# Optimization experiments

Measured on AMD Instinct MI355X. Metric: run time of the kernel, lower is better.

## Reference

```python
import jax, jax.numpy as jnp
import numpy as np

HEADS = 4
LN_EPS = 1e-5

def layernorm(x, w, b):
    m = x.mean(-1, keepdims=True)
    v = ((x - m) ** 2).mean(-1, keepdims=True)
    return (x - m) * jax.lax.rsqrt(v + LN_EPS) * w + b

def conv3d(x, w, b, pad, dil=1, groups=1):
    out = jax.lax.conv_general_dilated(
        x, w, (1, 1, 1), [(pad, pad)] * 3,
        rhs_dilation=(dil, dil, dil),
        dimension_numbers=('NCDHW', 'OIDHW', 'NCDHW'),
        feature_group_count=groups)
    return out + b[None, :, None, None, None]

def trilinear_gather(x_flat, pz, py, px, D, H, W):
    # x_flat: [B,C,S]; pz/py/px: [B,S] fractional sample coords, zero padding outside
    z0f, y0f, x0f = jnp.floor(pz), jnp.floor(py), jnp.floor(px)
    wz, wy, wx = pz - z0f, py - y0f, px - x0f
    z0, y0, x0 = z0f.astype(jnp.int32), y0f.astype(jnp.int32), x0f.astype(jnp.int32)
    acc = jnp.zeros_like(x_flat)
    for dz in (0, 1):
        for dy in (0, 1):
            for dx in (0, 1):
                iz, iy, ix = z0 + dz, y0 + dy, x0 + dx
                cw = (wz if dz else 1.0 - wz) * (wy if dy else 1.0 - wy) * (wx if dx else 1.0 - wx)
                valid = (iz >= 0) & (iz < D) & (iy >= 0) & (iy < H) & (ix >= 0) & (ix < W)
                idx = (jnp.clip(iz, 0, D - 1) * H + jnp.clip(iy, 0, H - 1)) * W + jnp.clip(ix, 0, W - 1)
                vals = jnp.take_along_axis(x_flat, idx[:, None, :], axis=2)
                acc = acc + vals * (cw * valid)[:, None, :]
    return acc

def deform_conv3d(x, off_w, off_b, w, b):
    # DeformConvPack: offsets from a regular 3x3x3 conv, then offset trilinear sampling + conv
    B, C, D, H, W = x.shape
    K = 27
    offsets = conv3d(x, off_w, off_b, 1).reshape(B, K, 3, D * H * W)
    gz, gy, gx = jnp.indices((D, H, W))
    bz = gz.reshape(-1).astype(x.dtype)[None]
    by = gy.reshape(-1).astype(x.dtype)[None]
    bx = gx.reshape(-1).astype(x.dtype)[None]
    x_flat = x.reshape(B, C, -1)
    O = w.shape[0]
    wk = w.reshape(O, C, K)
    out = jnp.zeros((B, O, D * H * W), x.dtype)
    for k in range(K):  # fixed 27 kernel taps
        kz, ky, kx = k // 9, (k // 3) % 3, k % 3
        pz = bz + (kz - 1) + offsets[:, k, 0]
        py = by + (ky - 1) + offsets[:, k, 1]
        px = bx + (kx - 1) + offsets[:, k, 2]
        samp = trilinear_gather(x_flat, pz, py, px, D, H, W)  # [B,C,S]
        out = out + jnp.einsum('bcs,oc->bos', samp, wk[:, :, k])
    out = out + b[None, :, None]
    return out.reshape(B, O, D, H, W)

def forward(x, temperature, qkv_w, norm_w, norm_b, proj1_w, proj1_b, conv0_w, conv0_b,
            convsp_w, convsp_b, off_w, off_b, dcn_w, dcn_b, conv1_w, conv1_b,
            proj2_w, proj2_b, norm2_w, norm2_b, out_w, out_b, H, W, D):
    B, N, C = x.shape
    hd = C // HEADS
    qkv = (x @ qkv_w.T).reshape(B, N, 3, HEADS, hd).transpose(2, 0, 3, 1, 4)  # [3,B,h,N,hd]
    q = qkv[0].transpose(0, 1, 3, 2)  # [B,h,hd,N]
    k = qkv[1].transpose(0, 1, 3, 2)
    v = qkv[2].transpose(0, 1, 3, 2)
    q = q / jnp.maximum(jnp.sqrt((q * q).sum(-1, keepdims=True)), 1e-12)
    k = k / jnp.maximum(jnp.sqrt((k * k).sum(-1, keepdims=True)), 1e-12)
    attn = jnp.einsum('bhcn,bhdn->bhcd', q, k) * temperature[None]
    attn = jax.nn.softmax(attn, axis=-1)
    x_ca = jnp.einsum('bhcd,bhdn->bhcn', attn, v).transpose(0, 3, 1, 2).reshape(B, N, C)
    x_ca = layernorm(x_ca, norm_w, norm_b)
    x5 = x_ca.transpose(0, 2, 1).reshape(B, C, H, W, D)
    shortcut = x5
    y = jnp.einsum('bcxyz,oc->boxyz', x5, proj1_w) + proj1_b[None, :, None, None, None]
    y = jax.nn.gelu(y, approximate=False)
    u = y
    a = conv3d(y, conv0_w, conv0_b, 2, 1, C)      # depthwise k=5 pad=2
    a = conv3d(a, convsp_w, convsp_b, 9, 3, C)    # depthwise k=7 pad=9 dil=3
    a = deform_conv3d(a, off_w, off_b, dcn_w, dcn_b)
    a = jnp.einsum('bcxyz,oc->boxyz', a, conv1_w) + conv1_b[None, :, None, None, None]
    y = u * a
    y = jnp.einsum('bcxyz,oc->boxyz', y, proj2_w) + proj2_b[None, :, None, None, None]
    y = y + shortcut
    x_sa = y.reshape(B, C, N).transpose(0, 2, 1)           # lka returns [B,N,C]
    x_sa = x_sa.reshape(B, C, N).transpose(0, 2, 1)        # faithful torch reshape-after-permute
    x_sa = layernorm(x_sa, norm2_w, norm2_b)
    return x_sa @ out_w.T + out_b

def setup_inputs():
    key = jax.random.key(0)
    ks = jax.random.split(key, 12)
    B, C, H, W, D = 2, 64, 32, 32, 32
    N = H * W * D
    s = 0.02
    return dict(
        x=jax.random.normal(ks[0], (B, N, C), jnp.float32),
        temperature=jnp.ones((HEADS, 1, 1), jnp.float32),
        qkv_w=jax.random.normal(ks[1], (3 * C, C), jnp.float32) * s,
        norm_w=jnp.ones((C,), jnp.float32), norm_b=jnp.zeros((C,), jnp.float32),
        proj1_w=jax.random.normal(ks[2], (C, C), jnp.float32) * s,
        proj1_b=jnp.zeros((C,), jnp.float32),
        conv0_w=jax.random.normal(ks[3], (C, 1, 5, 5, 5), jnp.float32) * s,
        conv0_b=jnp.zeros((C,), jnp.float32),
        convsp_w=jax.random.normal(ks[4], (C, 1, 7, 7, 7), jnp.float32) * s,
        convsp_b=jnp.zeros((C,), jnp.float32),
        off_w=jax.random.normal(ks[5], (81, C, 3, 3, 3), jnp.float32) * 0.01,
        off_b=jnp.zeros((81,), jnp.float32),
        dcn_w=jax.random.normal(ks[6], (C, C, 3, 3, 3), jnp.float32) * s,
        dcn_b=jnp.zeros((C,), jnp.float32),
        conv1_w=jax.random.normal(ks[7], (C, C), jnp.float32) * s,
        conv1_b=jnp.zeros((C,), jnp.float32),
        proj2_w=jax.random.normal(ks[8], (C, C), jnp.float32) * s,
        proj2_b=jnp.zeros((C,), jnp.float32),
        norm2_w=jnp.ones((C,), jnp.float32), norm2_b=jnp.zeros((C,), jnp.float32),
        out_w=jax.random.normal(ks[9], (C, C), jnp.float32) * s,
        out_b=jnp.zeros((C,), jnp.float32),
        B_in=B, C_in=C, H=H, W=W, D=D,
    )

def reference(x, temperature, qkv_w, norm_w, norm_b, proj1_w, proj1_b, conv0_w, conv0_b,
              convsp_w, convsp_b, off_w, off_b, dcn_w, dcn_b, conv1_w, conv1_b,
              proj2_w, proj2_b, norm2_w, norm2_b, out_w, out_b, B_in, C_in, H, W, D):
    return forward(x, temperature, qkv_w, norm_w, norm_b, proj1_w, proj1_b, conv0_w, conv0_b,
                   convsp_w, convsp_b, off_w, off_b, dcn_w, dcn_b, conv1_w, conv1_b,
                   proj2_w, proj2_b, norm2_w, norm2_b, out_w, out_b, H, W, D)
```

## Files before the change

### kernel.cpp

```cpp
#include <hip/hip_runtime.h>
#include <hip/hip_bf16.h>

#define S 32768
#define BUFN (2*64*32768)

typedef __bf16 v8bf __attribute__((ext_vector_type(8)));
typedef float v4f __attribute__((ext_vector_type(4)));
typedef int v4i __attribute__((ext_vector_type(4)));

__device__ __forceinline__ ushort f2b(float f) {
  union { float f; unsigned u; } v; v.f = f;
  unsigned r = (v.u + 0x7fffu + ((v.u >> 16) & 1u)) >> 16;
  return (ushort)r;
}
__device__ __forceinline__ float b2f(ushort h) {
  union { unsigned u; float f; } v; v.u = ((unsigned)h) << 16;
  return v.f;
}
__device__ __forceinline__ float u2f(unsigned u) {
  union { unsigned u; float f; } v; v.u = u;
  return v.f;
}
__device__ __forceinline__ v8bf pack8(const float* f) {
  v4i d;
#pragma unroll
  for (int m = 0; m < 4; m++)
    d[m] = (int)((unsigned)f2b(f[2*m]) | ((unsigned)f2b(f[2*m+1]) << 16));
  return __builtin_bit_cast(v8bf, d);
}

__global__ void k_wt(const float* __restrict__ offw, const float* __restrict__ dcnw,
                     const float* __restrict__ qkvw, const float* __restrict__ p1w,
                     const float* __restrict__ c1w, const float* __restrict__ p2w,
                     ushort* __restrict__ wt_off16, ushort* __restrict__ wt_dcn16,
                     ushort* __restrict__ qkv16, ushort* __restrict__ p1w16,
                     ushort* __restrict__ c1w16, ushort* __restrict__ p2w16) {
  int i = blockIdx.x*256 + threadIdx.x;
  if (i < 27*96*64) {
    int c = i & 63, o = (i >> 6) % 96, t = i / 6144;
    wt_off16[i] = (o < 81) ? f2b(offw[o*1728 + c*27 + t]) : (ushort)0;
  }
  if (i < 27*64*64) {
    int c = i & 63, o = (i >> 6) & 63, k = i >> 12;
    wt_dcn16[i] = f2b(dcnw[(o*64 + c)*27 + k]);
  }
  if (i < 12288) qkv16[i] = f2b(qkvw[i]);
  if (i < 4096) {
    p1w16[i] = f2b(p1w[i]);
    c1w16[i] = f2b(c1w[i]);
    p2w16[i] = f2b(p2w[i]);
  }
}

__global__ __launch_bounds__(256) void k_qkv(const float* __restrict__ x,
    const ushort* __restrict__ qkvw16, float* __restrict__ q,
    float* __restrict__ k, float* __restrict__ v) {
  int bi = blockIdx.x;
  int b = bi >> 9, tile = bi & 511;
  int tid = threadIdx.x;
  int lane = tid & 63, wv = tid >> 6;
  int si = lane & 15, rq = lane >> 4, q8 = rq << 3;
  int s = (tile << 6) + (wv << 4) + si;
  const float* xr = x + ((size_t)(b*S + s) << 6);
  float4 t0 = *(const float4*)(xr + q8);
  float4 t1 = *(const float4*)(xr + q8 + 4);
  float4 t2 = *(const float4*)(xr + q8 + 32);
  float4 t3 = *(const float4*)(xr + q8 + 36);
  float f0[8] = {t0.x,t0.y,t0.z,t0.w,t1.x,t1.y,t1.z,t1.w};
  float f1[8] = {t2.x,t2.y,t2.z,t2.w,t3.x,t3.y,t3.z,t3.w};
  v8bf b0 = pack8(f0);
  v8bf b1 = pack8(f1);
  v4f acc[12];
#pragma unroll
  for (int t = 0; t < 12; t++) acc[t] = (v4f){0.f,0.f,0.f,0.f};
#pragma unroll
  for (int t = 0; t < 12; t++) {
    const ushort* ap = qkvw16 + (((t<<4) + si) << 6) + q8;
    v8bf a0 = *(const v8bf*)ap;
    v8bf a1 = *(const v8bf*)(ap + 32);
    acc[t] = __builtin_amdgcn_mfma_f32_16x16x32_bf16(a0, b0, acc[t], 0,0,0);
    acc[t] = __builtin_amdgcn_mfma_f32_16x16x32_bf16(a1, b1, acc[t], 0,0,0);
  }
#pragma unroll
  for (int t = 0; t < 12; t++) {
    float* dst = (t < 4) ? q : (t < 8 ? k : v);
    int chb = (t & 3) << 4;
#pragma unroll
    for (int r = 0; r < 4; r++) {
      int ch = chb + rq*4 + r;
      dst[((size_t)(b*64 + ch))*S + s] = acc[t][r];
    }
  }
}

__global__ __launch_bounds__(256) void k_rownorm(const float* __restrict__ q,
    const float* __restrict__ k, float* __restrict__ inv) {
  int row = blockIdx.x;
  const float* p = (row < 128) ? (q + (size_t)row*S) : (k + (size_t)(row-128)*S);
  const float4* p4 = (const float4*)p;
  float ss = 0.f;
  for (int i = threadIdx.x; i < S/4; i += 256) {
    float4 t = p4[i];
    ss += t.x*t.x + t.y*t.y + t.z*t.z + t.w*t.w;
  }
  __shared__ float red[256];
  red[threadIdx.x] = ss; __syncthreads();
  for (int st = 128; st > 0; st >>= 1) {
    if (threadIdx.x < st) red[threadIdx.x] += red[threadIdx.x+st];
    __syncthreads();
  }
  if (threadIdx.x == 0) inv[row] = 1.0f / fmaxf(sqrtf(red[0]), 1e-12f);
}

__global__ __launch_bounds__(256) void k_gram(const float* __restrict__ q,
    const float* __restrict__ k, float* __restrict__ gram) {
  int bi = blockIdx.x;
  int b = bi >> 8, h = (bi >> 6) & 3, chunk = bi & 63;
  int tid = threadIdx.x;
  int lane = tid & 63, wv = tid >> 6;
  int si = lane & 15, rq = lane >> 4, q8 = rq << 3;
  const float* qb = q + ((size_t)(b*64 + h*16 + si))*S;
  const float* kb = k + ((size_t)(b*64 + h*16 + si))*S;
  int n0 = chunk*512 + wv*128;
  v4f acc = (v4f){0.f,0.f,0.f,0.f};
#pragma unroll
  for (int st = 0; st < 4; st++) {
    int n = n0 + st*32 + q8;
    float4 qa = *(const float4*)(qb + n);
    float4 qc = *(const float4*)(qb + n + 4);
    float4 ka = *(const float4*)(kb + n);
    float4 kc = *(const float4*)(kb + n + 4);
    float fq[8] = {qa.x,qa.y,qa.z,qa.w,qc.x,qc.y,qc.z,qc.w};
    float fk[8] = {ka.x,ka.y,ka.z,ka.w,kc.x,kc.y,kc.z,kc.w};
    v8bf a0 = pack8(fq);
    v8bf b0 = pack8(fk);
    acc = __builtin_amdgcn_mfma_f32_16x16x32_bf16(a0, b0, acc, 0,0,0);
  }
#pragma unroll
  for (int r = 0; r < 4; r++) {
    int c = rq*4 + r;
    atomicAdd(&gram[((b*4+h)*16 + c)*16 + si], acc[r]);
  }
}

__global__ __launch_bounds__(256) void k_xca_ln(const float* __restrict__ v,
    const float* __restrict__ gram, const float* __restrict__ inv,
    const float* __restrict__ temp,
    const float* __restrict__ nw, const float* __restrict__ nb,
    float* __restrict__ x5) {
  __shared__ float at[1024];
  __shared__ float wsh[64], bsh[64];
  int gid = blockIdx.x*256 + threadIdx.x;
  int b = gid >> 15, n = gid & (S-1);
  int tid = threadIdx.x;
  if (tid < 64) {
    int h = tid >> 4, c = tid & 15;
    float iq = inv[b*64 + h*16 + c];
    float tp = temp[h];
    float l[16], m = -1e30f;
#pragma unroll
    for (int d = 0; d < 16; d++) {
      float vv = gram[((b*4+h)*16+c)*16 + d] * iq * inv[128 + b*64 + h*16 + d] * tp;
      l[d] = vv; m = fmaxf(m, vv);
    }
    float s = 0.f;
#pragma unroll
    for (int d = 0; d < 16; d++) { l[d] = expf(l[d]-m); s += l[d]; }
    float is = 1.0f / s;
#pragma unroll
    for (int d = 0; d < 16; d++) at[(h*16+c)*16 + d] = l[d]*is;
  } else if (tid < 128) {
    wsh[tid-64] = nw[tid-64]; bsh[tid-64] = nb[tid-64];
  }
  __syncthreads();
  const float* vb = v + (size_t)b*64*S + n;
  float vv[64];
#pragma unroll
  for (int ch = 0; ch < 64; ch++) vv[ch] = vb[(size_t)ch*S];
  float xc[64];
#pragma unroll
  for (int h = 0; h < 4; h++)
#pragma unroll
    for (int cc = 0; cc < 16; cc++) {
      float a = 0.f;
#pragma unroll
      for (int d = 0; d < 16; d++) a += at[(h*16+cc)*16 + d] * vv[h*16+d];
      xc[h*16+cc] = a;
    }
  float mean = 0.f;
#pragma unroll
  for (int ch = 0; ch < 64; ch++) mean += xc[ch];
  mean *= (1.0f/64.0f);
  float var = 0.f;
#pragma unroll
  for (int ch = 0; ch < 64; ch++) { float d = xc[ch]-mean; var += d*d; }
  var *= (1.0f/64.0f);
  float rs = rsqrtf(var + 1e-5f);
  float* xb = x5 + (size_t)b*64*S + n;
#pragma unroll
  for (int ch = 0; ch < 64; ch++)
    xb[(size_t)ch*S] = (xc[ch]-mean)*rs*wsh[ch] + bsh[ch];
}

__global__ __launch_bounds__(256) void k_proj1(const float* __restrict__ x5,
    const ushort* __restrict__ p1w16, const float* __restrict__ bias, float* __restrict__ u) {
  int bi = blockIdx.x;
  int b = bi >> 9, tile = bi & 511;
  int tid = threadIdx.x;
  int lane = tid & 63, wv = tid >> 6;
  int si = lane & 15, rq = lane >> 4, q8 = rq << 3;
  int s = (tile << 6) + (wv << 4) + si;
  const float* xb = x5 + ((size_t)b << 21) + s;
  float f0[8], f1[8];
#pragma unroll
  for (int j = 0; j < 8; j++) {
    f0[j] = xb[(size_t)(q8 + j) << 15];
    f1[j] = xb[(size_t)(32 + q8 + j) << 15];
  }
  v8bf b0 = pack8(f0);
  v8bf b1 = pack8(f1);
  v4f acc[4];
#pragma unroll
  for (int t = 0; t < 4; t++) acc[t] = (v4f){0.f,0.f,0.f,0.f};
#pragma unroll
  for (int t = 0; t < 4; t++) {
    const ushort* ap = p1w16 + (((t<<4) + si) << 6) + q8;
    v8bf a0 = *(const v8bf*)ap;
    v8bf a1 = *(const v8bf*)(ap + 32);
    acc[t] = __builtin_amdgcn_mfma_f32_16x16x32_bf16(a0, b0, acc[t], 0,0,0);
    acc[t] = __builtin_amdgcn_mfma_f32_16x16x32_bf16(a1, b1, acc[t], 0,0,0);
  }
  float* ub = u + ((size_t)b << 21) + s;
#pragma unroll
  for (int t = 0; t < 4; t++)
#pragma unroll
    for (int r = 0; r < 4; r++) {
      int ch = (t << 4) + rq*4 + r;
      float a = acc[t][r] + bias[ch];
      float g = 0.5f*a*(1.0f + erff(a*0.70710678118654752f));
      ub[(size_t)ch << 15] = g;
    }
}

__global__ __launch_bounds__(256) void k_conv0(const float* __restrict__ in,
    const float* __restrict__ w, const float* __restrict__ bias, ushort* __restrict__ out) {
  __shared__ ushort tile[5*32*40];
  __shared__ float wsh[128];
  int bi = blockIdx.x;
  int z = bi & 31, c = (bi >> 5) & 63, b = bi >> 11;
  const float* ib = in + ((size_t)(b*64+c) << 15);
  for (int i = threadIdx.x; i < 800; i += 256)
    ((int4*)tile)[i] = make_int4(0,0,0,0);
  if (threadIdx.x < 125) wsh[threadIdx.x] = w[c*125 + threadIdx.x];
  __syncthreads();
  for (int i = threadIdx.x; i < 5*1024; i += 256) {
    int dz = i >> 10, r = i & 1023;
    int zg = z + dz - 2;
    if (zg >= 0 && zg < 32)
      tile[(dz*32 + (r >> 5))*40 + (r & 31) + 2] = f2b(ib[zg*1024 + r]);
  }
  __syncthreads();
  int y = threadIdx.x >> 3, x0 = (threadIdx.x & 7) << 2;
  float bv = bias[c];
  float acc[4] = {bv, bv, bv, bv};
  for (int dz = 0; dz < 5; dz++) {
#pragma unroll
    for (int dy = 0; dy < 5; dy++) {
      int yy = y + dy - 2;
      if (yy < 0 || yy >= 32) continue;
      const float* wp = &wsh[(dz*5+dy)*5];
      float wreg[5];
#pragma unroll
      for (int dx = 0; dx < 5; dx++) wreg[dx] = wp[dx];
      const ushort* rp = &tile[(dz*32+yy)*40 + x0];
      int2 rl = *(const int2*)rp;
      int2 rh = *(const int2*)(rp + 4);
      float row[8];
      row[0]=u2f(((unsigned)rl.x)<<16); row[1]=u2f(rl.x & 0xffff0000u);
      row[2]=u2f(((unsigned)rl.y)<<16); row[3]=u2f(rl.y & 0xffff0000u);
      row[4]=u2f(((unsigned)rh.x)<<16); row[5]=u2f(rh.x & 0xffff0000u);
      row[6]=u2f(((unsigned)rh.y)<<16); row[7]=u2f(rh.y & 0xffff0000u);
#pragma unroll
      for (int dx = 0; dx < 5; dx++)
#pragma unroll
        for (int j = 0; j < 4; j++)
          acc[j] += wreg[dx] * row[dx+j];
    }
  }
  ushort* ob = out + ((size_t)(b*64+c) << 15) + z*1024 + y*32 + x0;
  unsigned p0 = (unsigned)f2b(acc[0]) | ((unsigned)f2b(acc[1]) << 16);
  unsigned p1 = (unsigned)f2b(acc[2]) | ((unsigned)f2b(acc[3]) << 16);
  *(int2*)ob = make_int2((int)p0, (int)p1);
}

__global__ __launch_bounds__(256) void k_convsp(const ushort* __restrict__ in,
    const float* __restrict__ w, const float* __restrict__ bias, ushort* __restrict__ out) {
  __shared__ ushort tile[7*32*56];
  __shared__ float wsh[344];
  int bi = blockIdx.x;
  int z = bi & 31, c = (bi >> 5) & 63, b = bi >> 11;
  const ushort* ib = in + ((size_t)(b*64+c) << 15);
  for (int i = threadIdx.x; i < 1568; i += 256)
    ((int4*)tile)[i] = make_int4(0,0,0,0);
  for (int i = threadIdx.x; i < 343; i += 256) wsh[i] = w[c*343 + i];
  __syncthreads();
  for (int i = threadIdx.x; i < 7*1024; i += 256) {
    int t = i >> 10, r = i & 1023;
    int zg = z + 3*t - 9;
    if (zg >= 0 && zg < 32)
      tile[(t*32 + (r >> 5))*56 + (r & 31) + 9] = ib[zg*1024 + r];
  }
  __syncthreads();
  int y = threadIdx.x >> 3, x0 = (threadIdx.x & 7) << 2;
  float bv = bias[c];
  float acc[4] = {bv, bv, bv, bv};
  for (int t = 0; t < 7; t++) {
#pragma unroll
    for (int dy = 0; dy < 7; dy++) {
      int yy = y + 3*dy - 9;
      if (yy < 0 || yy >= 32) continue;
      const float* wp = &wsh[(t*7+dy)*7];
      float wreg[7];
#pragma unroll
      for (int dx = 0; dx < 7; dx++) wreg[dx] = wp[dx];
      const ushort* rp = &tile[(t*32+yy)*56 + x0];
      float row[24];
#pragma unroll
      for (int qq = 0; qq < 6; qq++) {
        int2 rv = *(const int2*)(rp + 4*qq);
        row[4*qq+0]=u2f(((unsigned)rv.x)<<16); row[4*qq+1]=u2f(rv.x & 0xffff0000u);
        row[4*qq+2]=u2f(((unsigned)rv.y)<<16); row[4*qq+3]=u2f(rv.y & 0xffff0000u);
      }
#pragma unroll
      for (int dx = 0; dx < 7; dx++)
#pragma unroll
        for (int j = 0; j < 4; j++)
          acc[j] += wreg[dx] * row[3*dx+j];
    }
  }
  ushort* ob = out + ((size_t)(b*64+c) << 15) + z*1024 + y*32 + x0;
  unsigned p0 = (unsigned)f2b(acc[0]) | ((unsigned)f2b(acc[1]) << 16);
  unsigned p1 = (unsigned)f2b(acc[2]) | ((unsigned)f2b(acc[3]) << 16);
  *(int2*)ob = make_int2((int)p0, (int)p1);
}

__global__ __launch_bounds__(256) void k_tr(const ushort* __restrict__ a2,
                                            ushort* __restrict__ a2t) {
  __shared__ ushort tile[64*66];
  int bi = blockIdx.x;
  int b = bi >> 9, chunk = bi & 511;
  int s0 = chunk << 6;
  const ushort* ib = a2 + ((size_t)b << 21) + s0;
#pragma unroll
  for (int i = 0; i < 16; i++) {
    int j = threadIdx.x + (i << 8);
    int c = j >> 6, sl = j & 63;
    tile[c*66 + sl] = ib[((size_t)c << 15) + sl];
  }
  __syncthreads();
  ushort* ob = a2t + ((size_t)b << 21) + ((size_t)s0 << 6);
#pragma unroll
  for (int i = 0; i < 16; i++) {
    int j = threadIdx.x + (i << 8);
    int sl = j >> 6, c = j & 63;
    ob[sl*64 + c] = tile[c*66 + sl];
  }
}

__global__ __launch_bounds__(256) void k_offconv(const ushort* __restrict__ a2t,
    const ushort* __restrict__ wt16, float* __restrict__ off) {
  int bi = blockIdx.x;
  int b = bi >> 9, tile = bi & 511;
  int s0 = tile << 6;
  int tid = threadIdx.x;
  int lane = tid & 63, wv = tid >> 6;
  int si = lane & 15, rq = lane >> 4, q8 = rq << 3;
  int sw = s0 + (wv << 4);
  int s_c = sw + si;
  int zc = s_c >> 10, yc = (s_c >> 5) & 31, xc = s_c & 31;
  const ushort* a2b = a2t + ((size_t)b << 21);
  v4f acc[6];
#pragma unroll
  for (int i = 0; i < 6; i++) acc[i] = (v4f){0.f,0.f,0.f,0.f};
  const v4i z4 = {0,0,0,0};
  for (int t = 0; t < 27; t++) {
    int kz = t/9, ky = (t/3)%3, kx = t%3;
    int zz = zc + kz - 1, yy = yc + ky - 1, xx = xc + kx - 1;
    bool ok = (zz>=0 && zz<32 && yy>=0 && yy<32 && xx>=0 && xx<32);
    v8bf b0 = __builtin_bit_cast(v8bf, z4);
    v8bf b1 = __builtin_bit_cast(v8bf, z4);
    if (ok) {
      const ushort* p = a2b + ((size_t)((zz<<10)+(yy<<5)+xx) << 6) + q8;
      b0 = *(const v8bf*)p;
      b1 = *(const v8bf*)(p + 32);
    }
    const ushort* wk = wt16 + t*6144;
#pragma unroll
    for (int ot = 0; ot < 6; ot++) {
      const ushort* ap = wk + (((ot<<4) + si) << 6) + q8;
      v8bf a0 = *(const v8bf*)ap;
      v8bf a1 = *(const v8bf*)(ap + 32);
      acc[ot] = __builtin_amdgcn_mfma_f32_16x16x32_bf16(a0, b0, acc[ot], 0,0,0);
      acc[ot] = __builtin_amdgcn_mfma_f32_16x16x32_bf16(a1, b1, acc[ot], 0,0,0);
    }
  }
#pragma unroll
  for (int ot = 0; ot < 6; ot++)
#pragma unroll
    for (int r = 0; r < 4; r++) {
      int o = ot*16 + rq*4 + r;
      if (o < 81)
        off[(((size_t)(b*81 + o)) << 15) + sw + si] = acc[ot][r];
    }
}

__global__ __launch_bounds__(256) void k_dcn(const ushort* __restrict__ a2t,
    const float* __restrict__ off, const float* __restrict__ off_b,
    const ushort* __restrict__ wt16, float* __restrict__ out) {
  __shared__ float ofs[81*66];
  __shared__ ushort scr[4][16*72];
  int bi = blockIdx.x;
  int b = bi >> 9, tile = bi & 511;
  int s0 = tile << 6;
  int tid = threadIdx.x;
  const float* offbase = off + (((size_t)(b*81)) << 15) + s0;
  for (int i = tid; i < 5184; i += 256) {
    int r = i >> 6, sl = i & 63;
    ofs[r*66 + sl] = offbase[((size_t)r << 15) + sl] + off_b[r];
  }
  __syncthreads();
  int lane = tid & 63, wv = tid >> 6;
  int sr = lane >> 3, cs = lane & 7;
  int si = lane & 15, rq = lane >> 4;
  int sw = s0 + (wv << 4);
  const ushort* a2b = a2t + ((size_t)b << 21);
  ushort* myscr = &scr[wv][0];
  int sA = sw + sr, sB = sw + 8 + sr;
  int zA = sA >> 10, yA = (sA >> 5) & 31, xA = sA & 31;
  int zB = sB >> 10, yB = (sB >> 5) & 31, xB = sB & 31;
  int slcA = (wv << 4) + sr, slcB = slcA + 8;
  v4f acc[4];
#pragma unroll
  for (int t = 0; t < 4; t++) acc[t] = (v4f){0.f,0.f,0.f,0.f};
  for (int k = 0; k < 27; k++) {
    int kz = k/9, ky = (k/3)%3, kx = k%3;
    int idxA[8], idxB[8];
    float wA[8], wB[8];
    {
      float pz = (float)(zA + kz - 1) + ofs[(3*k+0)*66 + slcA];
      float py = (float)(yA + ky - 1) + ofs[(3*k+1)*66 + slcA];
      float px = (float)(xA + kx - 1) + ofs[(3*k+2)*66 + slcA];
      float fz = floorf(pz), fy = floorf(py), fx = floorf(px);
      float wz = pz-fz, wy = py-fy, wx = px-fx;
      int z0 = (int)fz, y0 = (int)fy, x0 = (int)fx;
      int zi[2], yi[2], xi[2]; float zw[2], yw[2], xw[2];
#pragma unroll
      for (int d = 0; d < 2; d++) {
        int iz = z0 + d; zi[d] = min(max(iz,0),31) << 10;
        zw[d] = (iz >= 0 && iz < 32) ? (d ? wz : 1.f-wz) : 0.f;
        int iy = y0 + d; yi[d] = min(max(iy,0),31) << 5;
        yw[d] = (iy >= 0 && iy < 32) ? (d ? wy : 1.f-wy) : 0.f;
        int ix = x0 + d; xi[d] = min(max(ix,0),31);
        xw[d] = (ix >= 0 && ix < 32) ? (d ? wx : 1.f-wx) : 0.f;
      }
#pragma unroll
      for (int r = 0; r < 8; r++) {
        int dz = r >> 2, dy = (r >> 1) & 1, dx = r & 1;
        idxA[r] = zi[dz] + yi[dy] + xi[dx];
        wA[r] = zw[dz] * yw[dy] * xw[dx];
      }
    }
    {
      float pz = (float)(zB + kz - 1) + ofs[(3*k+0)*66 + slcB];
      float py = (float)(yB + ky - 1) + ofs[(3*k+1)*66 + slcB];
      float px = (float)(xB + kx - 1) + ofs[(3*k+2)*66 + slcB];
      float fz = floorf(pz), fy = floorf(py), fx = floorf(px);
      float wz = pz-fz, wy = py-fy, wx = px-fx;
      int z0 = (int)fz, y0 = (int)fy, x0 = (int)fx;
      int zi[2], yi[2], xi[2]; float zw[2], yw[2], xw[2];
#pragma unroll
      for (int d = 0; d < 2; d++) {
        int iz = z0 + d; zi[d] = min(max(iz,0),31) << 10;
        zw[d] = (iz >= 0 && iz < 32) ? (d ? wz : 1.f-wz) : 0.f;
        int iy = y0 + d; yi[d] = min(max(iy,0),31) << 5;
        yw[d] = (iy >= 0 && iy < 32) ? (d ? wy : 1.f-wy) : 0.f;
        int ix = x0 + d; xi[d] = min(max(ix,0),31);
        xw[d] = (ix >= 0 && ix < 32) ? (d ? wx : 1.f-wx) : 0.f;
      }
#pragma unroll
      for (int r = 0; r < 8; r++) {
        int dz = r >> 2, dy = (r >> 1) & 1, dx = r & 1;
        idxB[r] = zi[dz] + yi[dy] + xi[dx];
        wB[r] = zw[dz] * yw[dy] * xw[dx];
      }
    }
    v4i gA[8], gB[8];
#pragma unroll
    for (int r = 0; r < 8; r++)
      gA[r] = *(const v4i*)(a2b + ((size_t)idxA[r] << 6) + (cs << 3));
#pragma unroll
    for (int r = 0; r < 8; r++)
      gB[r] = *(const v4i*)(a2b + ((size_t)idxB[r] << 6) + (cs << 3));
    float faA[8], faB[8];
#pragma unroll
    for (int j = 0; j < 8; j++) { faA[j] = 0.f; faB[j] = 0.f; }
#pragma unroll
    for (int r = 0; r < 8; r++) {
      float wa = wA[r], wb = wB[r];
#pragma unroll
      for (int m = 0; m < 4; m++) {
        unsigned da = (unsigned)gA[r][m];
        faA[2*m]   += wa * u2f(da << 16);
        faA[2*m+1] += wa * u2f(da & 0xffff0000u);
        unsigned db = (unsigned)gB[r][m];
        faB[2*m]   += wb * u2f(db << 16);
        faB[2*m+1] += wb * u2f(db & 0xffff0000u);
      }
    }
    v4i dA, dB;
#pragma unroll
    for (int m = 0; m < 4; m++) {
      unsigned l0 = (__float_as_uint(faA[2*m])   + 0x8000u) >> 16;
      unsigned h0 = (__float_as_uint(faA[2*m+1]) + 0x8000u) & 0xffff0000u;
      dA[m] = (int)(l0 | h0);
      unsigned l1 = (__float_as_uint(faB[2*m])   + 0x8000u) >> 16;
      unsigned h1 = (__float_as_uint(faB[2*m+1]) + 0x8000u) & 0xffff0000u;
      dB[m] = (int)(l1 | h1);
    }
    *(v4i*)&myscr[sr*72 + (cs << 3)]       = dA;
    *(v4i*)&myscr[(8+sr)*72 + (cs << 3)]   = dB;
    v8bf bf0 = *(const v8bf*)&myscr[si*72 + (rq << 3)];
    v8bf bf1 = *(const v8bf*)&myscr[si*72 + 32 + (rq << 3)];
    const ushort* wk = wt16 + (k << 12);
#pragma unroll
    for (int ot = 0; ot < 4; ot++) {
      const ushort* ap = wk + (((ot<<4) + si) << 6) + (rq << 3);
      v8bf a0 = *(const v8bf*)ap;
      v8bf a1 = *(const v8bf*)(ap + 32);
      acc[ot] = __builtin_amdgcn_mfma_f32_16x16x32_bf16(a0, bf0, acc[ot], 0,0,0);
      acc[ot] = __builtin_amdgcn_mfma_f32_16x16x32_bf16(a1, bf1, acc[ot], 0,0,0);
    }
  }
#pragma unroll
  for (int ot = 0; ot < 4; ot++)
#pragma unroll
    for (int r = 0; r < 4; r++) {
      int o = (ot << 4) + rq*4 + r;
      out[(((size_t)(b*64 + o)) << 15) + sw + si] = acc[ot][r];
    }
}

__global__ __launch_bounds__(256) void k_fuse2(const float* __restrict__ dcn0,
    const float* __restrict__ dcn_b, const ushort* __restrict__ c1w16,
    const float* __restrict__ c1b, const float* __restrict__ u,
    const ushort* __restrict__ p2w16, const float* __restrict__ p2b,
    const float* __restrict__ x5, float* __restrict__ y2) {
  __shared__ ushort scr[4][16*72];
  int bi = blockIdx.x;
  int b = bi >> 9, tile = bi & 511;
  int tid = threadIdx.x;
  int lane = tid & 63, wv = tid >> 6;
  int si = lane & 15, rq = lane >> 4, q8 = rq << 3;
  int s = (tile << 6) + (wv << 4) + si;
  ushort* myscr = &scr[wv][0];
  const float* db = dcn0 + ((size_t)b << 21) + s;
  float f0[8], f1[8];
#pragma unroll
  for (int j = 0; j < 8; j++) {
    f0[j] = db[(size_t)(q8 + j) << 15]      + dcn_b[q8 + j];
    f1[j] = db[(size_t)(32 + q8 + j) << 15] + dcn_b[32 + q8 + j];
  }
  v8bf b0 = pack8(f0);
  v8bf b1 = pack8(f1);
  v4f acc1[4];
#pragma unroll
  for (int t = 0; t < 4; t++) acc1[t] = (v4f){0.f,0.f,0.f,0.f};
#pragma unroll
  for (int t = 0; t < 4; t++) {
    const ushort* ap = c1w16 + (((t<<4) + si) << 6) + q8;
    v8bf a0 = *(const v8bf*)ap;
    v8bf a1 = *(const v8bf*)(ap + 32);
    acc1[t] = __builtin_amdgcn_mfma_f32_16x16x32_bf16(a0, b0, acc1[t], 0,0,0);
    acc1[t] = __builtin_amdgcn_mfma_f32_16x16x32_bf16(a1, b1, acc1[t], 0,0,0);
  }
  const float* ub = u + ((size_t)b << 21) + s;
#pragma unroll
  for (int t = 0; t < 4; t++)
#pragma unroll
    for (int r = 0; r < 4; r++) {
      int o = (t << 4) + rq*4 + r;
      float m = ub[(size_t)o << 15] * (acc1[t][r] + c1b[o]);
      myscr[si*72 + o] = f2b(m);
    }
  v8bf m0 = *(const v8bf*)&myscr[si*72 + q8];
  v8bf m1 = *(const v8bf*)&myscr[si*72 + 32 + q8];
  v4f acc2[4];
#pragma unroll
  for (int t = 0; t < 4; t++) acc2[t] = (v4f){0.f,0.f,0.f,0.f};
#pragma unroll
  for (int t = 0; t < 4; t++) {
    const ushort* ap = p2w16 + (((t<<4) + si) << 6) + q8;
    v8bf a0 = *(const v8bf*)ap;
    v8bf a1 = *(const v8bf*)(ap + 32);
    acc2[t] = __builtin_amdgcn_mfma_f32_16x16x32_bf16(a0, m0, acc2[t], 0,0,0);
    acc2[t] = __builtin_amdgcn_mfma_f32_16x16x32_bf16(a1, m1, acc2[t], 0,0,0);
  }
  const float* sb = x5 + ((size_t)b << 21) + s;
  float* yb = y2 + ((size_t)b << 21) + s;
#pragma unroll
  for (int t = 0; t < 4; t++)
#pragma unroll
    for (int r = 0; r < 4; r++) {
      int o = (t << 4) + rq*4 + r;
      yb[(size_t)o << 15] = acc2[t][r] + p2b[o] + sb[(size_t)o << 15];
    }
}

__global__ __launch_bounds__(256) void k_final(const float* __restrict__ y2,
    const float* __restrict__ n2w, const float* __restrict__ n2b,
    const float* __restrict__ ow, const float* __restrict__ ob, float* __restrict__ out) {
  __shared__ float wsh[4096];
  __shared__ float nw[64], nb[64], obs[64];
  int bi = blockIdx.x;
  int b = bi >> 7; int mg = (bi >> 4) & 7; int r0 = (bi & 15)*4;
  for (int i = threadIdx.x; i < 4096; i += 256) wsh[i] = ow[i];
  if (threadIdx.x < 64) {
    nw[threadIdx.x]=n2w[threadIdx.x]; nb[threadIdx.x]=n2b[threadIdx.x];
    obs[threadIdx.x]=ob[threadIdx.x];
  }
  __syncthreads();
  int mi = threadIdx.x & 63, rg = threadIdx.x >> 6;
  int r = r0 + rg;
  int m = mg*64 + mi;
  int n = m*64 + r;
  const float* yb = y2 + ((size_t)(b*64+r))*S + m;
  float v[64];
#pragma unroll
  for (int c = 0; c < 64; c++) v[c] = yb[(size_t)c*512];
  float mean = 0.f;
#pragma unroll
  for (int c = 0; c < 64; c++) mean += v[c];
  mean *= (1.0f/64.0f);
  float var = 0.f;
#pragma unroll
  for (int c = 0; c < 64; c++) { float d = v[c]-mean; var += d*d; }
  var *= (1.0f/64.0f);
  float rs = rsqrtf(var + 1e-5f);
#pragma unroll
  for (int c = 0; c < 64; c++) v[c] = (v[c]-mean)*rs*nw[c] + nb[c];
  float* orow = out + ((size_t)b*S + n)*64;
  for (int o4 = 0; o4 < 16; o4++) {
    const float4* w0 = (const float4*)&wsh[(o4*4+0)*64];
    const float4* w1 = (const float4*)&wsh[(o4*4+1)*64];
    const float4* w2 = (const float4*)&wsh[(o4*4+2)*64];
    const float4* w3 = (const float4*)&wsh[(o4*4+3)*64];
    float t0=obs[o4*4+0], t1=obs[o4*4+1], t2=obs[o4*4+2], t3=obs[o4*4+3];
#pragma unroll
    for (int c4 = 0; c4 < 16; c4++) {
      float4 a0 = w0[c4], a1 = w1[c4], a2 = w2[c4], a3 = w3[c4];
      float v0 = v[4*c4], v1 = v[4*c4+1], v2 = v[4*c4+2], v3 = v[4*c4+3];
      t0 += a0.x*v0 + a0.y*v1 + a0.z*v2 + a0.w*v3;
      t1 += a1.x*v0 + a1.y*v1 + a1.z*v2 + a1.w*v3;
      t2 += a2.x*v0 + a2.y*v1 + a2.z*v2 + a2.w*v3;
      t3 += a3.x*v0 + a3.y*v1 + a3.z*v2 + a3.w*v3;
    }
    float4 a; a.x=t0; a.y=t1; a.z=t2; a.w=t3;
    ((float4*)orow)[o4] = a;
  }
}

extern "C" void kernel_launch(void* const* d_in, const int* in_sizes, int n_in,
                              void* d_out, int out_size, void* d_ws, size_t ws_size,
                              hipStream_t stream) {
  const float* x      = (const float*)d_in[0];
  const float* temp   = (const float*)d_in[1];
  const float* qkv_w  = (const float*)d_in[2];
  const float* norm_w = (const float*)d_in[3];
  const float* norm_b = (const float*)d_in[4];
  const float* p1w    = (const float*)d_in[5];
  const float* p1b    = (const float*)d_in[6];
  const float* c0w    = (const float*)d_in[7];
  const float* c0b    = (const float*)d_in[8];
  const float* cspw   = (const float*)d_in[9];
  const float* cspb   = (const float*)d_in[10];
  const float* offw   = (const float*)d_in[11];
  const float* offb   = (const float*)d_in[12];
  const float* dcnw   = (const float*)d_in[13];
  const float* dcnb   = (const float*)d_in[14];
  const float* c1w    = (const float*)d_in[15];
  const float* c1b    = (const float*)d_in[16];
  const float* p2w    = (const float*)d_in[17];
  const float* p2b    = (const float*)d_in[18];
  const float* n2w    = (const float*)d_in[19];
  const float* n2b    = (const float*)d_in[20];
  const float* outw   = (const float*)d_in[21];
  const float* outb   = (const float*)d_in[22];
  float* out = (float*)d_out;

  float* Wa  = (float*)d_ws;
  float* Wb  = Wa + BUFN;
  float* Wc  = Wb + BUFN;
  float* OFF = Wc + BUFN;
  float* SM  = OFF + (size_t)2*81*S;
  float* SM_inv  = SM;
  float* SM_gram = SM + 256;
  ushort* WT_OFF16 = (ushort*)(SM + 4352);
  ushort* WT_DCN16 = WT_OFF16 + 165888;
  ushort* QKV16    = WT_DCN16 + 110592;
  ushort* P1W16    = QKV16 + 12288;
  ushort* C1W16    = P1W16 + 4096;
  ushort* P2W16    = C1W16 + 4096;
  float* vbuf = out;
  ushort* A1_16 = (ushort*)d_out;
  ushort* A2_16 = (ushort*)Wc;
  ushort* a2t = (ushort*)d_out;

  hipMemsetAsync(SM, 0, 4352*sizeof(float), stream);
  k_wt     <<<648, 256, 0, stream>>>(offw, dcnw, qkv_w, p1w, c1w, p2w,
                                     WT_OFF16, WT_DCN16, QKV16, P1W16, C1W16, P2W16);

  k_qkv    <<<1024,256, 0, stream>>>(x, QKV16, Wa, Wb, vbuf);
  k_rownorm<<<256, 256, 0, stream>>>(Wa, Wb, SM_inv);
  k_gram   <<<512, 256, 0, stream>>>(Wa, Wb, SM_gram);
  k_xca_ln <<<256, 256, 0, stream>>>(vbuf, SM_gram, SM_inv, temp, norm_w, norm_b, Wa);
  k_proj1  <<<1024,256, 0, stream>>>(Wa, P1W16, p1b, Wb);
  k_conv0  <<<4096,256, 0, stream>>>(Wb, c0w, c0b, A1_16);
  k_convsp <<<4096,256, 0, stream>>>(A1_16, cspw, cspb, A2_16);
  k_tr     <<<1024,256, 0, stream>>>(A2_16, a2t);
  k_offconv<<<1024,256, 0, stream>>>(a2t, WT_OFF16, OFF);
  k_dcn    <<<1024,256, 0, stream>>>(a2t, OFF, offb, WT_DCN16, Wc);
  k_fuse2  <<<1024,256, 0, stream>>>(Wc, dcnb, C1W16, c1b, Wb, P2W16, p2b, Wa, OFF);
  k_final  <<<256, 256, 0, stream>>>(OFF, n2w, n2b, outw, outb, out);
}
```

Measured before the change: 733.8 us.

## Fuse row norms into gram kernel and proj1 into XCA-LN kernel

Row sum-of-squares for q and k are now accumulated inside the gram kernel through shuffles and atomics, which removes the separate rownorm pass over q and k. The proj1 GEMM+GELU is fused into the XCA+LayerNorm kernel: normalized values are staged as bf16 in shared memory and fed straight to MFMA, so x5 is not re-read from global. The memset is folded into the weight-conversion kernel. Risks are extra shared memory (about 37KB) lowering occupancy and a larger register footprint. The x5 output is still written, possibly for a later residual.

```diff
diff --git a/kernel.cpp b/kernel.cpp
--- a/kernel.cpp
+++ b/kernel.cpp
@@ -34,7 +34,8 @@
                      const float* __restrict__ c1w, const float* __restrict__ p2w,
                      ushort* __restrict__ wt_off16, ushort* __restrict__ wt_dcn16,
                      ushort* __restrict__ qkv16, ushort* __restrict__ p1w16,
-                     ushort* __restrict__ c1w16, ushort* __restrict__ p2w16) {
+                     ushort* __restrict__ c1w16, ushort* __restrict__ p2w16,
+                     float* __restrict__ sm) {
   int i = blockIdx.x*256 + threadIdx.x;
   if (i < 27*96*64) {
     int c = i & 63, o = (i >> 6) % 96, t = i / 6144;
@@ -50,6 +51,7 @@
     c1w16[i] = f2b(c1w[i]);
     p2w16[i] = f2b(p2w[i]);
   }
+  if (i < 4352) sm[i] = 0.f;
 }
 
 __global__ __launch_bounds__(256) void k_qkv(const float* __restrict__ x,
@@ -93,27 +95,9 @@
   }
 }
 
-__global__ __launch_bounds__(256) void k_rownorm(const float* __restrict__ q,
-    const float* __restrict__ k, float* __restrict__ inv) {
-  int row = blockIdx.x;
-  const float* p = (row < 128) ? (q + (size_t)row*S) : (k + (size_t)(row-128)*S);
-  const float4* p4 = (const float4*)p;
-  float ss = 0.f;
-  for (int i = threadIdx.x; i < S/4; i += 256) {
-    float4 t = p4[i];
-    ss += t.x*t.x + t.y*t.y + t.z*t.z + t.w*t.w;
-  }
-  __shared__ float red[256];
-  red[threadIdx.x] = ss; __syncthreads();
-  for (int st = 128; st > 0; st >>= 1) {
-    if (threadIdx.x < st) red[threadIdx.x] += red[threadIdx.x+st];
-    __syncthreads();
-  }
-  if (threadIdx.x == 0) inv[row] = 1.0f / fmaxf(sqrtf(red[0]), 1e-12f);
-}
-
 __global__ __launch_bounds__(256) void k_gram(const float* __restrict__ q,
-    const float* __restrict__ k, float* __restrict__ gram) {
+    const float* __restrict__ k, float* __restrict__ gram, float* __restrict__ ss) {
+  __shared__ float redq[4][16], redk[4][16];
   int bi = blockIdx.x;
   int b = bi >> 8, h = (bi >> 6) & 3, chunk = bi & 63;
   int tid = threadIdx.x;
@@ -123,6 +107,7 @@
   const float* kb = k + ((size_t)(b*64 + h*16 + si))*S;
   int n0 = chunk*512 + wv*128;
   v4f acc = (v4f){0.f,0.f,0.f,0.f};
+  float sq = 0.f, sk = 0.f;
 #pragma unroll
   for (int st = 0; st < 4; st++) {
     int n = n0 + st*32 + q8;
@@ -132,10 +117,24 @@
     float4 kc = *(const float4*)(kb + n + 4);
     float fq[8] = {qa.x,qa.y,qa.z,qa.w,qc.x,qc.y,qc.z,qc.w};
     float fk[8] = {ka.x,ka.y,ka.z,ka.w,kc.x,kc.y,kc.z,kc.w};
+#pragma unroll
+    for (int j = 0; j < 8; j++) { sq += fq[j]*fq[j]; sk += fk[j]*fk[j]; }
     v8bf a0 = pack8(fq);
     v8bf b0 = pack8(fk);
     acc = __builtin_amdgcn_mfma_f32_16x16x32_bf16(a0, b0, acc, 0,0,0);
   }
+  sq += __shfl_xor(sq, 16); sq += __shfl_xor(sq, 32);
+  sk += __shfl_xor(sk, 16); sk += __shfl_xor(sk, 32);
+  if (rq == 0) { redq[wv][si] = sq; redk[wv][si] = sk; }
+  __syncthreads();
+  if (tid < 16)
+    atomicAdd(&ss[b*64 + h*16 + tid],
+              redq[0][tid]+redq[1][tid]+redq[2][tid]+redq[3][tid]);
+  else if (tid < 32) {
+    int t = tid - 16;
+    atomicAdd(&ss[128 + b*64 + h*16 + t],
+              redk[0][t]+redk[1][t]+redk[2][t]+redk[3][t]);
+  }
 #pragma unroll
   for (int r = 0; r < 4; r++) {
     int c = rq*4 + r;
@@ -143,24 +142,27 @@
   }
 }
 
-__global__ __launch_bounds__(256) void k_xca_ln(const float* __restrict__ v,
-    const float* __restrict__ gram, const float* __restrict__ inv,
+__global__ __launch_bounds__(256) void k_xca_proj(const float* __restrict__ v,
+    const float* __restrict__ gram, const float* __restrict__ ss,
     const float* __restrict__ temp,
     const float* __restrict__ nw, const float* __restrict__ nb,
-    float* __restrict__ x5) {
+    const ushort* __restrict__ p1w16, const float* __restrict__ p1b,
+    float* __restrict__ x5, float* __restrict__ u) {
   __shared__ float at[1024];
   __shared__ float wsh[64], bsh[64];
+  __shared__ ushort xsh[4][64*72];
   int gid = blockIdx.x*256 + threadIdx.x;
   int b = gid >> 15, n = gid & (S-1);
   int tid = threadIdx.x;
   if (tid < 64) {
     int h = tid >> 4, c = tid & 15;
-    float iq = inv[b*64 + h*16 + c];
+    float iq = 1.0f / fmaxf(sqrtf(ss[b*64 + h*16 + c]), 1e-12f);
     float tp = temp[h];
     float l[16], m = -1e30f;
 #pragma unroll
     for (int d = 0; d < 16; d++) {
-      float vv = gram[((b*4+h)*16+c)*16 + d] * iq * inv[128 + b*64 + h*16 + d] * tp;
+      float id = 1.0f / fmaxf(sqrtf(ss[128 + b*64 + h*16 + d]), 1e-12f);
+      float vv = gram[((b*4+h)*16+c)*16 + d] * iq * id * tp;
       l[d] = vv; m = fmaxf(m, vv);
     }
     float s = 0.f;
@@ -197,49 +199,51 @@
   var *= (1.0f/64.0f);
   float rs = rsqrtf(var + 1e-5f);
   float* xb = x5 + (size_t)b*64*S + n;
-#pragma unroll
-  for (int ch = 0; ch < 64; ch++)
-    xb[(size_t)ch*S] = (xc[ch]-mean)*rs*wsh[ch] + bsh[ch];
-}
-
-__global__ __launch_bounds__(256) void k_proj1(const float* __restrict__ x5,
-    const ushort* __restrict__ p1w16, const float* __restrict__ bias, float* __restrict__ u) {
-  int bi = blockIdx.x;
-  int b = bi >> 9, tile = bi & 511;
-  int tid = threadIdx.x;
   int lane = tid & 63, wv = tid >> 6;
+  ushort* myrow = &xsh[wv][lane*72];
+#pragma unroll
+  for (int ch = 0; ch < 64; ch++) {
+    float val = (xc[ch]-mean)*rs*wsh[ch] + bsh[ch];
+    xc[ch] = val;
+    xb[(size_t)ch*S] = val;
+  }
+#pragma unroll
+  for (int c8 = 0; c8 < 8; c8++) {
+    v4i d;
+#pragma unroll
+    for (int m = 0; m < 4; m++)
+      d[m] = (int)((unsigned)f2b(xc[c8*8+2*m]) | ((unsigned)f2b(xc[c8*8+2*m+1]) << 16));
+    *(v4i*)&myrow[c8*8] = d;
+  }
   int si = lane & 15, rq = lane >> 4, q8 = rq << 3;
-  int s = (tile << 6) + (wv << 4) + si;
-  const float* xb = x5 + ((size_t)b << 21) + s;
-  float f0[8], f1[8];
-#pragma unroll
-  for (int j = 0; j < 8; j++) {
-    f0[j] = xb[(size_t)(q8 + j) << 15];
-    f1[j] = xb[(size_t)(32 + q8 + j) << 15];
-  }
-  v8bf b0 = pack8(f0);
-  v8bf b1 = pack8(f1);
-  v4f acc[4];
-#pragma unroll
-  for (int t = 0; t < 4; t++) acc[t] = (v4f){0.f,0.f,0.f,0.f};
-#pragma unroll
-  for (int t = 0; t < 4; t++) {
-    const ushort* ap = p1w16 + (((t<<4) + si) << 6) + q8;
-    v8bf a0 = *(const v8bf*)ap;
-    v8bf a1 = *(const v8bf*)(ap + 32);
-    acc[t] = __builtin_amdgcn_mfma_f32_16x16x32_bf16(a0, b0, acc[t], 0,0,0);
-    acc[t] = __builtin_amdgcn_mfma_f32_16x16x32_bf16(a1, b1, acc[t], 0,0,0);
-  }
-  float* ub = u + ((size_t)b << 21) + s;
-#pragma unroll
-  for (int t = 0; t < 4; t++)
-#pragma unroll
-    for (int r = 0; r < 4; r++) {
-      int ch = (t << 4) + rq*4 + r;
-      float a = acc[t][r] + bias[ch];
-      float g = 0.5f*a*(1.0f + erff(a*0.70710678118654752f));
-      ub[(size_t)ch << 15] = g;
-    }
+  int nbase = (blockIdx.x & 127)*256 + wv*64;
+  float* ub = u + ((size_t)b << 21);
+#pragma unroll
+  for (int sub = 0; sub < 4; sub++) {
+    v8bf bf0 = *(const v8bf*)&xsh[wv][(sub*16 + si)*72 + q8];
+    v8bf bf1 = *(const v8bf*)&xsh[wv][(sub*16 + si)*72 + 32 + q8];
+    v4f acc[4];
+#pragma unroll
+    for (int t = 0; t < 4; t++) acc[t] = (v4f){0.f,0.f,0.f,0.f};
+#pragma unroll
+    for (int t = 0; t < 4; t++) {
+      const ushort* ap = p1w16 + (((t<<4) + si) << 6) + q8;
+      v8bf a0 = *(const v8bf*)ap;
+      v8bf a1 = *(const v8bf*)(ap + 32);
+      acc[t] = __builtin_amdgcn_mfma_f32_16x16x32_bf16(a0, bf0, acc[t], 0,0,0);
+      acc[t] = __builtin_amdgcn_mfma_f32_16x16x32_bf16(a1, bf1, acc[t], 0,0,0);
+    }
+    int sgl = nbase + sub*16 + si;
+#pragma unroll
+    for (int t = 0; t < 4; t++)
+#pragma unroll
+      for (int r = 0; r < 4; r++) {
+        int ch = (t << 4) + rq*4 + r;
+        float a = acc[t][r] + p1b[ch];
+        float g = 0.5f*a*(1.0f + erff(a*0.70710678118654752f));
+        ub[((size_t)ch << 15) + sgl] = g;
+      }
+  }
 }
 
 __global__ __launch_bounds__(256) void k_conv0(const float* __restrict__ in,
@@ -702,7 +706,7 @@
   float* Wc  = Wb + BUFN;
   float* OFF = Wc + BUFN;
   float* SM  = OFF + (size_t)2*81*S;
-  float* SM_inv  = SM;
+  float* SM_ss   = SM;
   float* SM_gram = SM + 256;
   ushort* WT_OFF16 = (ushort*)(SM + 4352);
   ushort* WT_DCN16 = WT_OFF16 + 165888;
@@ -715,20 +719,18 @@
   ushort* A2_16 = (ushort*)Wc;
   ushort* a2t = (ushort*)d_out;
 
-  hipMemsetAsync(SM, 0, 4352*sizeof(float), stream);
   k_wt     <<<648, 256, 0, stream>>>(offw, dcnw, qkv_w, p1w, c1w, p2w,
-                                     WT_OFF16, WT_DCN16, QKV16, P1W16, C1W16, P2W16);
-
-  k_qkv    <<<1024,256, 0, stream>>>(x, QKV16, Wa, Wb, vbuf);
-  k_rownorm<<<256, 256, 0, stream>>>(Wa, Wb, SM_inv);
-  k_gram   <<<512, 256, 0, stream>>>(Wa, Wb, SM_gram);
-  k_xca_ln <<<256, 256, 0, stream>>>(vbuf, SM_gram, SM_inv, temp, norm_w, norm_b, Wa);
-  k_proj1  <<<1024,256, 0, stream>>>(Wa, P1W16, p1b, Wb);
-  k_conv0  <<<4096,256, 0, stream>>>(Wb, c0w, c0b, A1_16);
-  k_convsp <<<4096,256, 0, stream>>>(A1_16, cspw, cspb, A2_16);
-  k_tr     <<<1024,256, 0, stream>>>(A2_16, a2t);
-  k_offconv<<<1024,256, 0, stream>>>(a2t, WT_OFF16, OFF);
-  k_dcn    <<<1024,256, 0, stream>>>(a2t, OFF, offb, WT_DCN16, Wc);
-  k_fuse2  <<<1024,256, 0, stream>>>(Wc, dcnb, C1W16, c1b, Wb, P2W16, p2b, Wa, OFF);
-  k_final  <<<256, 256, 0, stream>>>(OFF, n2w, n2b, outw, outb, out);
-}
+                                     WT_OFF16, WT_DCN16, QKV16, P1W16, C1W16, P2W16, SM);
+
+  k_qkv     <<<1024,256, 0, stream>>>(x, QKV16, Wa, Wb, vbuf);
+  k_gram    <<<512, 256, 0, stream>>>(Wa, Wb, SM_gram, SM_ss);
+  k_xca_proj<<<256, 256, 0, stream>>>(vbuf, SM_gram, SM_ss, temp, norm_w, norm_b,
+                                      P1W16, p1b, Wa, Wb);
+  k_conv0   <<<4096,256, 0, stream>>>(Wb, c0w, c0b, A1_16);
+  k_convsp  <<<4096,256, 0, stream>>>(A1_16, cspw, cspb, A2_16);
+  k_tr      <<<1024,256, 0, stream>>>(A2_16, a2t);
+  k_offconv <<<1024,256, 0, stream>>>(a2t, WT_OFF16, OFF);
+  k_dcn     <<<1024,256, 0, stream>>>(a2t, OFF, offb, WT_DCN16, Wc);
+  k_fuse2   <<<1024,256, 0, stream>>>(Wc, dcnb, C1W16, c1b, Wb, P2W16, p2b, Wa, OFF);
+  k_final   <<<256, 256, 0, stream>>>(OFF, n2w, n2b, outw, outb, out);
+}
```

Result: faster. 716.9 us (-2.3%).
